# Kernel optimization log

Hardware: AMD Instinct MI355X
Metric: run time of the kernel (lower is better)

## Reference

```python
import jax, jax.numpy as jnp
import numpy as np

DIVISOR = 2.0
NEGATIVE_SLOPE = 0.01


def setup_inputs() -> dict:
    key = jax.random.key(0)
    k1, k2, k3 = jax.random.split(key, 3)
    x = jax.random.normal(k1, (32, 128, 130, 130), dtype=jnp.float32)
    weight = jax.random.normal(k2, (256, 128, 3, 3), dtype=jnp.float32) * 0.05
    bias = jax.random.normal(k3, (256,), dtype=jnp.float32)
    return {"x": x, "weight": weight, "bias": bias}


def reference(x, weight, bias):
    # conv2d, stride=1, padding=0 (VALID), NCHW / OIHW layout
    y = jax.lax.conv_general_dilated(
        x, weight,
        window_strides=(1, 1),
        padding='VALID',
        dimension_numbers=('NCHW', 'OIHW', 'NCHW'),
    )
    y = y + bias[None, :, None, None]
    y = y * (1.0 / DIVISOR)
    # fused LeakyReLU epilogue
    return jnp.where(y >= 0, y, y * NEGATIVE_SLOPE)
```

## Files before the change

kernel.cpp:

```cpp
#include <hip/hip_runtime.h>
#include <hip/hip_bf16.h>
#include <stdint.h>

typedef __bf16 bf16x8 __attribute__((ext_vector_type(8)));
typedef float  f32x4  __attribute__((ext_vector_type(4)));

#define NSLOPE 0.01f

#define NB   32
#define CIN  128
#define HIN  130
#define WIN  130
#define KOUT 256
#define POUT 128
#define QOUT 128
#define HWIN (HIN*WIN)

#define XP_BYTES 138444800ull
#define WP_ELEMS (2*3*3*KOUT*64)

#define WS_BYTES 32768
#define XS_BYTES 33280
#define XS_BASE  65536
#define LDS_TOTAL 132096

__device__ __forceinline__ unsigned short f2bf(float f) {
    unsigned u = __builtin_bit_cast(unsigned, f);
    u += 0x7FFFu + ((u >> 16) & 1u);
    return (unsigned short)(u >> 16);
}

__device__ __forceinline__ void g2lds16(const void* g, void* l) {
    __builtin_amdgcn_global_load_lds(
        (const __attribute__((address_space(1))) void*)g,
        (__attribute__((address_space(3))) void*)l,
        16, 0, 0);
}

__global__ __launch_bounds__(256) void k_conv_x(const float* __restrict__ X,
                                                unsigned short* __restrict__ Xp) {
    __shared__ unsigned short tile[130*132];
    const int b = blockIdx.x;
    const int n = b / 130, h = b - n*130;
    const int tid = threadIdx.x;
    const size_t in_base = (size_t)n*(CIN*(size_t)HWIN) + (size_t)h*WIN;
    for (int fi = tid; fi < CIN*WIN; fi += 256) {
        int c = fi / WIN, w = fi - c*WIN;
        tile[w*132 + c] = f2bf(X[in_base + (size_t)c*HWIN + w]);
    }
    __syncthreads();
    unsigned short* outp = Xp + (size_t)b * (WIN*CIN);
    for (int oi = tid; oi < (WIN*CIN)/4; oi += 256) {
        int e = oi*4; int w = e >> 7; int c4 = e & 127;
        const unsigned short* t = &tile[w*132 + c4];
        ushort4 v; v.x = t[0]; v.y = t[1]; v.z = t[2]; v.w = t[3];
        *(ushort4*)(outp + e) = v;
    }
}

__global__ __launch_bounds__(256) void k_conv_w(const float* __restrict__ W,
                                                unsigned short* __restrict__ Wp) {
    int e = blockIdx.x*256 + threadIdx.x;
    if (e >= WP_ELEMS) return;
    int ci = e & 63;
    int k  = (e >> 6) & 255;
    int rsIdx = e >> 14;
    int cc = rsIdx / 9; int rem = rsIdx - cc*9; int r = rem / 3, s = rem - r*3;
    int c = cc*64 + ci;
    Wp[e] = f2bf(W[(size_t)k*1152 + (size_t)c*9 + r*3 + s]);
}

__device__ __forceinline__ void stage_w_half(const unsigned short* __restrict__ Wp,
                                             unsigned char* lds, int rsidx, int tid, int half) {
    const unsigned short* wbase = Wp + (size_t)rsidx * (KOUT*64);
    #pragma unroll
    for (int it = half*2; it < half*2 + 2; ++it) {
        const int t    = it*512 + tid;
        const int phys = t << 4;
        const int row  = phys >> 7;
        const int cib  = (phys & 127) ^ ((row & 7) << 4);
        g2lds16(wbase + (size_t)row*64 + (cib >> 1), lds + phys);
    }
}

__device__ __forceinline__ void stage_x(const unsigned short* __restrict__ Xp,
                                        unsigned char* lds, int n, int h0, int cc, int tid) {
    #pragma unroll
    for (int it = 0; it < 5; ++it) {
        const int t = it*512 + tid;
        if (t < 2080) {
            const int phys = t << 4;
            const int g    = phys >> 7;
            const int pl   = (g >= 130) ? 1 : 0;
            const int w    = g - 130*pl;
            const int cib  = (phys & 127) ^ ((g & 7) << 4);
            const unsigned short* src =
                Xp + ((size_t)((n*HIN + h0 + pl)*WIN + w))*CIN + cc*64 + (cib >> 1);
            g2lds16(src, lds + phys);
        }
    }
}

__global__ __launch_bounds__(512, 2) void k_conv_main(
    const unsigned short* __restrict__ Xp,
    const unsigned short* __restrict__ Wp,
    const float* __restrict__ bias,
    float* __restrict__ out)
{
    extern __shared__ __align__(16) unsigned char smem[];

    const int tid  = threadIdx.x;
    const int lane = tid & 63;
    const int wid  = tid >> 6;
    const int wm   = wid >> 2;
    const int wn   = wid & 3;
    const int l15  = lane & 15;
    const int kg   = lane >> 4;

    const int L     = ((blockIdx.x & 7) << 8) | (blockIdx.x >> 3);
    const int ppair = L & 63;
    const int n     = L >> 6;
    const int p2    = ppair << 1;

    f32x4 acc[8][4];
    #pragma unroll
    for (int i = 0; i < 8; ++i)
        #pragma unroll
        for (int j = 0; j < 4; ++j)
            acc[i][j] = (f32x4){0.f, 0.f, 0.f, 0.f};

    stage_w_half(Wp, smem, 0, tid, 0);
    stage_w_half(Wp, smem, 0, tid, 1);
    stage_x(Xp, smem + XS_BASE, n, p2, 0, tid);
    asm volatile("s_waitcnt vmcnt(0)" ::: "memory");
    __builtin_amdgcn_s_barrier();

    for (int t = 0; t < 18; ++t) {
        const int cc  = t / 9;
        const int rem = t - cc*9;
        const int s   = rem % 3;
        unsigned char* wsR = smem + (t & 1)*WS_BYTES;
        unsigned char* xsR = smem + XS_BASE + (((unsigned)t/3) & 1)*XS_BYTES;
        const int  tn    = t + 1;
        const bool haveW = (tn < 18);
        const bool haveX = haveW && (tn % 3 == 0);
        unsigned char* wsW = smem + (tn & 1)*WS_BYTES;
        unsigned char* xsW = smem + XS_BASE + (((unsigned)tn/3) & 1)*XS_BYTES;

        #pragma unroll
        for (int kq = 0; kq < 2; ++kq) {
            const int cib0 = kq*64 + kg*16;
            bf16x8 af[8], bx[4];
            #pragma unroll
            for (int mf = 0; mf < 8; ++mf) {
                const int row = wm*128 + mf*16 + l15;
                af[mf] = *(const bf16x8*)(wsR + row*128 + (cib0 ^ ((row & 7) << 4)));
            }
            #pragma unroll
            for (int nf = 0; nf < 4; ++nf) {
                const int qq   = wn*64 + nf*16 + l15;
                const int row2 = (qq >> 7)*130 + (qq & 127) + s;
                bx[nf] = *(const bf16x8*)(xsR + row2*128 + (cib0 ^ ((row2 & 7) << 4)));
            }
            if (haveW) stage_w_half(Wp, wsW, tn, tid, kq);
            if (kq == 1 && haveX) stage_x(Xp, xsW, n, p2 + (tn % 9) / 3, tn / 9, tid);

            __builtin_amdgcn_s_barrier();
            asm volatile("s_waitcnt lgkmcnt(0)" ::: "memory");
            __builtin_amdgcn_sched_barrier(0);
            __builtin_amdgcn_s_setprio(1);
            #pragma unroll
            for (int mf = 0; mf < 8; ++mf)
                #pragma unroll
                for (int nf = 0; nf < 4; ++nf)
                    acc[mf][nf] = __builtin_amdgcn_mfma_f32_16x16x32_bf16(
                        af[mf], bx[nf], acc[mf][nf], 0, 0, 0);
            __builtin_amdgcn_s_setprio(0);
            if (kq == 1)
                asm volatile("s_waitcnt vmcnt(0)" ::: "memory");
            __builtin_amdgcn_s_barrier();
        }
    }

    #pragma unroll
    for (int mf = 0; mf < 8; ++mf) {
        const int kb = wm*128 + mf*16 + kg*4;
        const float4 bv = *(const float4*)(bias + kb);
        const float bj[4] = {bv.x, bv.y, bv.z, bv.w};
        #pragma unroll
        for (int nf = 0; nf < 4; ++nf) {
            const int qq = wn*64 + nf*16 + l15;
            const int pl = qq >> 7, q = qq & 127;
            const size_t base = (((size_t)n*KOUT + kb)*POUT + (p2 + pl))*QOUT + q;
            #pragma unroll
            for (int j = 0; j < 4; ++j) {
                float y = (acc[mf][nf][j] + bj[j]) * 0.5f;
                out[base + (size_t)j*(POUT*QOUT)] = (y >= 0.f) ? y : y*NSLOPE;
            }
        }
    }
}

extern "C" void kernel_launch(void* const* d_in, const int* in_sizes, int n_in,
                              void* d_out, int out_size, void* d_ws, size_t ws_size,
                              hipStream_t stream) {
    const float* X = (const float*)d_in[0];
    const float* W = (const float*)d_in[1];
    const float* B = (const float*)d_in[2];
    float* out = (float*)d_out;
    unsigned short* Xp = (unsigned short*)d_ws;
    unsigned short* Wp = (unsigned short*)((char*)d_ws + XP_BYTES);

    (void)hipFuncSetAttribute((const void*)k_conv_main,
                              hipFuncAttributeMaxDynamicSharedMemorySize, LDS_TOTAL);

    k_conv_x   <<<NB*HIN, 256, 0, stream>>>(X, Xp);
    k_conv_w   <<<(WP_ELEMS + 255)/256, 256, 0, stream>>>(W, Wp);
    k_conv_main<<<2048, 512, LDS_TOTAL, stream>>>(Xp, Wp, B, out);
}
```

Baseline: 445.6 us.

## Stage four input rows once per channel chunk and split MFMA into halves

The input tile now holds all four rows needed by a 2-row output pair, loaded once per 64-channel chunk. Previously a 2-row tile was double-buffered and reloaded for each filter row, so this cuts redundant global-to-LDS input traffic and per-step X staging. The weight-fragment loads and MFMA block are split into two halves, with weight prefetch interleaved between them. The cost is an unoverlapped stall when the second channel chunk's input is loaded at t==8, plus extra barriers per iteration.

```diff
diff --git a/kernel.cpp b/kernel.cpp
--- a/kernel.cpp
+++ b/kernel.cpp
@@ -20,7 +20,6 @@
 #define WP_ELEMS (2*3*3*KOUT*64)
 
 #define WS_BYTES 32768
-#define XS_BYTES 33280
 #define XS_BASE  65536
 #define LDS_TOTAL 132096
 
@@ -83,19 +82,19 @@
     }
 }
 
-__device__ __forceinline__ void stage_x(const unsigned short* __restrict__ Xp,
-                                        unsigned char* lds, int n, int h0, int cc, int tid) {
-    #pragma unroll
-    for (int it = 0; it < 5; ++it) {
+__device__ __forceinline__ void stage_x4(const unsigned short* __restrict__ Xp,
+                                         unsigned char* lds, int n, int p2, int cc, int tid) {
+    #pragma unroll
+    for (int it = 0; it < 9; ++it) {
         const int t = it*512 + tid;
-        if (t < 2080) {
+        if (t < 4160) {
             const int phys = t << 4;
             const int g    = phys >> 7;
-            const int pl   = (g >= 130) ? 1 : 0;
-            const int w    = g - 130*pl;
+            const int rloc = g / 130;
+            const int w    = g - 130*rloc;
             const int cib  = (phys & 127) ^ ((g & 7) << 4);
             const unsigned short* src =
-                Xp + ((size_t)((n*HIN + h0 + pl)*WIN + w))*CIN + cc*64 + (cib >> 1);
+                Xp + ((size_t)((n*HIN + p2 + rloc)*WIN + w))*CIN + cc*64 + (cib >> 1);
             g2lds16(src, lds + phys);
         }
     }
@@ -122,6 +121,8 @@
     const int n     = L >> 6;
     const int p2    = ppair << 1;
 
+    unsigned char* xs = smem + XS_BASE;
+
     f32x4 acc[8][4];
     #pragma unroll
     for (int i = 0; i < 8; ++i)
@@ -131,53 +132,74 @@
 
     stage_w_half(Wp, smem, 0, tid, 0);
     stage_w_half(Wp, smem, 0, tid, 1);
-    stage_x(Xp, smem + XS_BASE, n, p2, 0, tid);
+    stage_x4(Xp, xs, n, p2, 0, tid);
     asm volatile("s_waitcnt vmcnt(0)" ::: "memory");
     __builtin_amdgcn_s_barrier();
 
     for (int t = 0; t < 18; ++t) {
         const int cc  = t / 9;
         const int rem = t - cc*9;
-        const int s   = rem % 3;
+        const int rr  = rem / 3;
+        const int s   = rem - rr*3;
         unsigned char* wsR = smem + (t & 1)*WS_BYTES;
-        unsigned char* xsR = smem + XS_BASE + (((unsigned)t/3) & 1)*XS_BYTES;
-        const int  tn    = t + 1;
-        const bool haveW = (tn < 18);
-        const bool haveX = haveW && (tn % 3 == 0);
-        unsigned char* wsW = smem + (tn & 1)*WS_BYTES;
-        unsigned char* xsW = smem + XS_BASE + (((unsigned)tn/3) & 1)*XS_BYTES;
+        const bool haveW   = (t + 1 < 18);
+        unsigned char* wsW = smem + ((t + 1) & 1)*WS_BYTES;
 
         #pragma unroll
         for (int kq = 0; kq < 2; ++kq) {
             const int cib0 = kq*64 + kg*16;
-            bf16x8 af[8], bx[4];
-            #pragma unroll
-            for (int mf = 0; mf < 8; ++mf) {
+            bf16x8 afA[4], afB[4], bx[4];
+
+            #pragma unroll
+            for (int mf = 0; mf < 4; ++mf) {
                 const int row = wm*128 + mf*16 + l15;
-                af[mf] = *(const bf16x8*)(wsR + row*128 + (cib0 ^ ((row & 7) << 4)));
+                afA[mf] = *(const bf16x8*)(wsR + row*128 + (cib0 ^ ((row & 7) << 4)));
             }
             #pragma unroll
             for (int nf = 0; nf < 4; ++nf) {
-                const int qq   = wn*64 + nf*16 + l15;
-                const int row2 = (qq >> 7)*130 + (qq & 127) + s;
-                bx[nf] = *(const bf16x8*)(xsR + row2*128 + (cib0 ^ ((row2 & 7) << 4)));
-            }
-            if (haveW) stage_w_half(Wp, wsW, tn, tid, kq);
-            if (kq == 1 && haveX) stage_x(Xp, xsW, n, p2 + (tn % 9) / 3, tn / 9, tid);
-
+                const int qq = wn*64 + nf*16 + l15;
+                const int g  = ((qq >> 7) + rr)*130 + (qq & 127) + s;
+                bx[nf] = *(const bf16x8*)(xs + g*128 + (cib0 ^ ((g & 7) << 4)));
+            }
+            if (haveW && kq == 0) stage_w_half(Wp, wsW, t + 1, tid, 0);
             __builtin_amdgcn_s_barrier();
             asm volatile("s_waitcnt lgkmcnt(0)" ::: "memory");
             __builtin_amdgcn_sched_barrier(0);
             __builtin_amdgcn_s_setprio(1);
             #pragma unroll
-            for (int mf = 0; mf < 8; ++mf)
+            for (int mf = 0; mf < 4; ++mf)
                 #pragma unroll
                 for (int nf = 0; nf < 4; ++nf)
                     acc[mf][nf] = __builtin_amdgcn_mfma_f32_16x16x32_bf16(
-                        af[mf], bx[nf], acc[mf][nf], 0, 0, 0);
+                        afA[mf], bx[nf], acc[mf][nf], 0, 0, 0);
+            __builtin_amdgcn_s_setprio(0);
+            __builtin_amdgcn_s_barrier();
+
+            #pragma unroll
+            for (int mf = 0; mf < 4; ++mf) {
+                const int row = wm*128 + (mf + 4)*16 + l15;
+                afB[mf] = *(const bf16x8*)(wsR + row*128 + (cib0 ^ ((row & 7) << 4)));
+            }
+            if (haveW && kq == 0) stage_w_half(Wp, wsW, t + 1, tid, 1);
+            __builtin_amdgcn_s_barrier();
+            asm volatile("s_waitcnt lgkmcnt(0)" ::: "memory");
+            __builtin_amdgcn_sched_barrier(0);
+            __builtin_amdgcn_s_setprio(1);
+            #pragma unroll
+            for (int mf = 0; mf < 4; ++mf)
+                #pragma unroll
+                for (int nf = 0; nf < 4; ++nf)
+                    acc[mf + 4][nf] = __builtin_amdgcn_mfma_f32_16x16x32_bf16(
+                        afB[mf], bx[nf], acc[mf + 4][nf], 0, 0, 0);
             __builtin_amdgcn_s_setprio(0);
             if (kq == 1)
                 asm volatile("s_waitcnt vmcnt(0)" ::: "memory");
+            __builtin_amdgcn_s_barrier();
+        }
+
+        if (t == 8) {
+            stage_x4(Xp, xs, n, p2, 1, tid);
+            asm volatile("s_waitcnt vmcnt(0)" ::: "memory");
             __builtin_amdgcn_s_barrier();
         }
     }
```

After: 444.5 us. About the same (-0.3%).
